# Optimization experiments

Measured on AMD Instinct MI355X. Metric: run time of the kernel, lower is better.

## Reference

```python
import jax, jax.numpy as jnp
import numpy as np

N, C, H, E = 10000, 128, 256, 320000
CUTOFF = 5.0
EPS = 1e-5


def _ln(x, g, b):
    mu = jnp.mean(x, axis=-1, keepdims=True)
    var = jnp.var(x, axis=-1, keepdims=True)
    return (x - mu) * jax.lax.rsqrt(var + EPS) * g + b


def setup_inputs() -> dict:
    key = jax.random.key(0)
    ks = jax.random.split(key, 24)

    def w(k, shape, fan_in):
        return (jax.random.normal(k, shape, dtype=jnp.float32) / np.sqrt(fan_in)).astype(jnp.float32)

    inp = {}
    inp["x"] = jax.random.normal(ks[0], (N, 3), dtype=jnp.float32)
    inp["h"] = jax.random.normal(ks[1], (N, C), dtype=jnp.float32)
    inp["edge_index"] = jax.random.randint(ks[2], (2, E), 0, N, dtype=jnp.int32)
    # edge_mlp: Linear(2C+1 -> H), SiLU, Linear(H -> H), SiLU
    inp["We1"] = w(ks[3], (2 * C + 1, H), 2 * C + 1); inp["be1"] = jnp.zeros((H,), jnp.float32)
    inp["We2"] = w(ks[4], (H, H), H);                inp["be2"] = jnp.zeros((H,), jnp.float32)
    # node_mlp: Linear(C+H -> H), SiLU, Linear(H -> C)
    inp["Wn1"] = w(ks[5], (C + H, H), C + H);        inp["bn1"] = jnp.zeros((H,), jnp.float32)
    inp["Wn2"] = w(ks[6], (H, C), H);                inp["bn2"] = jnp.zeros((C,), jnp.float32)
    # residual mlp: Linear(C -> H), SiLU, Dropout(eval), Linear(H -> C)
    inp["Wm1"] = w(ks[7], (C, H), C);                inp["bm1"] = jnp.zeros((H,), jnp.float32)
    inp["Wm2"] = w(ks[8], (H, C), H);                inp["bm2"] = jnp.zeros((C,), jnp.float32)
    # layernorms
    inp["g1"] = jnp.ones((C,), jnp.float32); inp["beta1"] = jnp.zeros((C,), jnp.float32)
    inp["g2"] = jnp.ones((C,), jnp.float32); inp["beta2"] = jnp.zeros((C,), jnp.float32)
    return inp


def reference(x, h, edge_index, We1, be1, We2, be2, Wn1, bn1, Wn2, bn2,
              Wm1, bm1, Wm2, bm2, g1, beta1, g2, beta2):
    row, col = edge_index[0], edge_index[1]

    h_res = h
    hn = _ln(h, g1, beta1)                              # [N, C]

    # ---- EGNN layer ----
    rel = x[row] - x[col]                               # [E, 3]
    dist = jnp.linalg.norm(rel, axis=-1, keepdims=True) # [E, 1]
    edge_in = jnp.concatenate([hn[row], hn[col], dist], axis=-1)  # [E, 2C+1]
    m = jax.nn.silu(edge_in @ We1 + be1)
    m = jax.nn.silu(m @ We2 + be2)                      # [E, H]

    d = dist[:, 0]
    Ccut = 0.5 * (jnp.cos(d * jnp.pi / CUTOFF) + 1.0)
    Ccut = Ccut * (d <= CUTOFF) * (d >= 0.0)
    m = m * Ccut[:, None]

    # mean-aggregate messages at target nodes (edge_index[1])
    sums = jax.ops.segment_sum(m, col, num_segments=N)          # [N, H]
    cnt = jax.ops.segment_sum(jnp.ones((m.shape[0],), m.dtype), col, num_segments=N)
    m_aggr = sums / jnp.maximum(cnt, 1.0)[:, None]

    hd = jax.nn.silu(jnp.concatenate([hn, m_aggr], axis=-1) @ Wn1 + bn1) @ Wn2 + bn2
    h_egnn = hn + hd

    h1 = h_res + h_egnn

    # ---- norm2 + MLP residual (dropout = identity in eval) ----
    h2 = _ln(h1, g2, beta2)
    h2 = jax.nn.silu(h2 @ Wm1 + bm1) @ Wm2 + bm2
    return h1 + h2
```

## Files before the change

### kernel.cpp

```cpp
#include <hip/hip_runtime.h>

#define NN 10000
#define CC 128
#define HH 256
#define EE 320000
#define ETILE 96
#define EBLOCKS 3334

typedef __bf16 bf16_t;
typedef __bf16 bf16x8 __attribute__((ext_vector_type(8)));
typedef __bf16 bf16x4 __attribute__((ext_vector_type(4)));
typedef float f32x4 __attribute__((ext_vector_type(4)));

__device__ __forceinline__ float silu_f(float v) {
#if __has_builtin(__builtin_amdgcn_rcpf)
  return v * __builtin_amdgcn_rcpf(1.0f + __expf(-v));
#else
  return v / (1.0f + __expf(-v));
#endif
}

template<int RE, int KD, int SA, int NT>
__device__ __forceinline__ void gemm_lg(const bf16_t* sAa, const bf16_t* __restrict__ BT,
                                        int nwavebase, int lr, int quad, f32x4 acc[RE][NT]) {
  for (int kk = 0; kk < KD; kk += 32) {
    bf16x8 a[RE]; bf16x8 b[NT];
#pragma unroll
    for (int re = 0; re < RE; re++)
      a[re] = *(const bf16x8*)(sAa + (re * 16 + lr) * SA + kk + quad * 8);
#pragma unroll
    for (int ce = 0; ce < NT; ce++)
      b[ce] = *(const bf16x8*)(BT + (size_t)(nwavebase + ce * 16 + lr) * KD + kk + quad * 8);
#pragma unroll
    for (int re = 0; re < RE; re++)
#pragma unroll
      for (int ce = 0; ce < NT; ce++)
        acc[re][ce] = __builtin_amdgcn_mfma_f32_16x16x32_bf16(a[re], b[ce], acc[re][ce], 0, 0, 0);
  }
}

__global__ __launch_bounds__(256) void prep_kernel(
    const float* __restrict__ We1, const float* __restrict__ We2,
    const float* __restrict__ Wn1, const float* __restrict__ Wn2,
    const float* __restrict__ Wm1, const float* __restrict__ Wm2,
    bf16_t* __restrict__ We1T, bf16_t* __restrict__ We2T,
    bf16_t* __restrict__ Wn1T, bf16_t* __restrict__ Wn2T,
    bf16_t* __restrict__ Wm1T, bf16_t* __restrict__ Wm2T,
    float* __restrict__ sums, int* __restrict__ cnt, uint4* __restrict__ edat) {
  int i = blockIdx.x * 256 + threadIdx.x;
  if (i < 327680) {
    const float* src; bf16_t* dst; int K, Nc, idx;
    if      (i < 65536)  { src = We1; dst = We1T; K = 256; Nc = 256; idx = i; }
    else if (i < 131072) { src = We2; dst = We2T; K = 256; Nc = 256; idx = i - 65536; }
    else if (i < 229376) { src = Wn1; dst = Wn1T; K = 384; Nc = 256; idx = i - 131072; }
    else if (i < 262144) { src = Wn2; dst = Wn2T; K = 256; Nc = 128; idx = i - 229376; }
    else if (i < 294912) { src = Wm1; dst = Wm1T; K = 128; Nc = 256; idx = i - 262144; }
    else                 { src = Wm2; dst = Wm2T; K = 256; Nc = 128; idx = i - 294912; }
    int n = idx / K, k = idx - n * K;
    dst[idx] = (bf16_t)src[(size_t)k * Nc + n];
  } else if (i < 327680 + 640000) {
    f32x4 z = {0.f, 0.f, 0.f, 0.f};
    ((f32x4*)sums)[i - 327680] = z;
  } else if (i < 327680 + 640000 + 2500) {
    int4 z = {0, 0, 0, 0};
    ((int4*)cnt)[i - 967680] = z;
  } else if (i < 327680 + 640000 + 2500 + 64) {
    uint4 z = {0u, 0u, 0u, 0u};
    edat[EE + (i - 970180)] = z;
  }
}

__global__ __launch_bounds__(256, 4) void node_pre_kernel(
    const float* __restrict__ h, const float* __restrict__ g1,
    const float* __restrict__ bt1,
    const bf16_t* __restrict__ We1T, const float* __restrict__ be1,
    bf16_t* __restrict__ hn16, bf16_t* __restrict__ PQ) {
  __shared__ __align__(16) bf16_t sHn[16 * 136];
  int tid = threadIdx.x;
  int lane = tid & 63, wave = tid >> 6;
  int lr = lane & 15, quad = lane >> 4;
  int n0 = blockIdx.x * 16;

  {
    int node = tid >> 4, c0 = (tid & 15) * 8;
    size_t base = (size_t)(n0 + node) * CC;
    f32x4 u0 = *(const f32x4*)(h + base + c0);
    f32x4 u1 = *(const f32x4*)(h + base + c0 + 4);
    float s = 0.f, sq = 0.f;
#pragma unroll
    for (int j = 0; j < 4; j++) { s += u0[j] + u1[j]; sq += u0[j] * u0[j] + u1[j] * u1[j]; }
#pragma unroll
    for (int o = 8; o > 0; o >>= 1) { s += __shfl_xor(s, o); sq += __shfl_xor(sq, o); }
    float mu = s * (1.0f / CC);
    float var = sq * (1.0f / CC) - mu * mu;
    float rs = rsqrtf(var + 1e-5f);
    f32x4 gg0 = *(const f32x4*)(g1 + c0), gg1 = *(const f32x4*)(g1 + c0 + 4);
    f32x4 bb0 = *(const f32x4*)(bt1 + c0), bb1 = *(const f32x4*)(bt1 + c0 + 4);
    bf16x8 ov;
#pragma unroll
    for (int j = 0; j < 4; j++) {
      ov[j] = (bf16_t)((u0[j] - mu) * rs * gg0[j] + bb0[j]);
      ov[j + 4] = (bf16_t)((u1[j] - mu) * rs * gg1[j] + bb1[j]);
    }
    *(bf16x8*)(sHn + node * 136 + c0) = ov;
    *(bf16x8*)(hn16 + base + c0) = ov;
  }
  __syncthreads();

  bool isQ = wave >= 2;
  int rbase = (wave & 1) * 128;
  int koff = isQ ? 128 : 0;
  f32x4 zf = {0.f, 0.f, 0.f, 0.f};
  f32x4 acc[8];
#pragma unroll
  for (int i = 0; i < 8; i++) acc[i] = zf;
  for (int kk = 0; kk < 128; kk += 32) {
    bf16x8 b = *(const bf16x8*)(sHn + lr * 136 + kk + quad * 8);
    bf16x8 a[8];
#pragma unroll
    for (int re = 0; re < 8; re++)
      a[re] = *(const bf16x8*)(We1T + (size_t)(rbase + re * 16 + lr) * 256 + koff + kk + quad * 8);
#pragma unroll
    for (int re = 0; re < 8; re++)
      acc[re] = __builtin_amdgcn_mfma_f32_16x16x32_bf16(a[re], b, acc[re], 0, 0, 0);
  }
#pragma unroll
  for (int re = 0; re < 8; re++) {
    int cb = rbase + re * 16 + quad * 4;
    f32x4 bb = isQ ? zf : *(const f32x4*)(be1 + cb);
    bf16x4 o;
#pragma unroll
    for (int r = 0; r < 4; r++) o[r] = (bf16_t)(acc[re][r] + bb[r]);
    *(bf16x4*)(PQ + (size_t)(n0 + lr) * 512 + (isQ ? 256 : 0) + cb) = o;
  }
}

__global__ __launch_bounds__(256) void count_kernel(const int* __restrict__ ei, int* __restrict__ cnt) {
  int e = blockIdx.x * 256 + threadIdx.x;
  atomicAdd(&cnt[ei[EE + e]], 1);
}

__global__ __launch_bounds__(1024) void scan_kernel(const int* __restrict__ cnt, int* __restrict__ cursor) {
  __shared__ int wsum[16];
  int tid = threadIdx.x, wave = tid >> 6, lane = tid & 63;
  int base = tid * 10;
  int v[10]; int S = 0;
#pragma unroll
  for (int j = 0; j < 10; j++) {
    int i = base + j;
    v[j] = (i < NN) ? cnt[i] : 0;
    S += v[j];
  }
  int s = S;
#pragma unroll
  for (int off = 1; off < 64; off <<= 1) { int t = __shfl_up(s, off); if (lane >= off) s += t; }
  if (lane == 63) wsum[wave] = s;
  __syncthreads();
  if (tid < 16) {
    int ws = wsum[tid];
#pragma unroll
    for (int off = 1; off < 16; off <<= 1) { int t = __shfl_up(ws, off); if (tid >= off) ws += t; }
    wsum[tid] = ws;
  }
  __syncthreads();
  int ex = ((wave > 0) ? wsum[wave - 1] : 0) + s - S;
#pragma unroll
  for (int j = 0; j < 10; j++) {
    int i = base + j;
    if (i < NN) cursor[i] = ex;
    ex += v[j];
  }
}

__global__ __launch_bounds__(256) void scatter_kernel(const int* __restrict__ ei,
                                                      const float* __restrict__ x,
                                                      int* __restrict__ cursor,
                                                      uint4* __restrict__ edat) {
  int e = blockIdx.x * 256 + threadIdx.x;
  int r = ei[e], c = ei[EE + e];
  float dx = x[3 * r] - x[3 * c];
  float dy = x[3 * r + 1] - x[3 * c + 1];
  float dz = x[3 * r + 2] - x[3 * c + 2];
  float d = sqrtf(dx * dx + dy * dy + dz * dz);
  float cc = (d <= 5.0f) ? 0.5f * (cosf(d * 0.6283185307179586f) + 1.0f) : 0.0f;
  int pos = atomicAdd(&cursor[c], 1);
  uint4 v = {(unsigned)r, (unsigned)c, __float_as_uint(d), __float_as_uint(cc)};
  edat[pos] = v;
}

__global__ __launch_bounds__(256, 3) void edge_mlp_kernel(
    const uint4* __restrict__ edat, const bf16_t* __restrict__ PQ,
    const float* __restrict__ We1last,
    const bf16_t* __restrict__ We2T, const float* __restrict__ be2,
    float* __restrict__ sums) {
  __shared__ __align__(16) bf16_t sM1[ETILE * 264];
  __shared__ int sRow[ETILE], sCol[ETILE];
  __shared__ float sD[ETILE], sCc[ETILE];
  __shared__ unsigned long long sMaskA;
  __shared__ unsigned sMaskB;
  int tid = threadIdx.x;
  int lane = tid & 63, wave = tid >> 6;
  int lr = lane & 15, quad = lane >> 4;
  int e0 = blockIdx.x * ETILE;

  if (tid < ETILE) {
    uint4 v = edat[e0 + tid];
    sRow[tid] = (int)v.x; sCol[tid] = (int)v.y;
    sD[tid] = __uint_as_float(v.z); sCc[tid] = __uint_as_float(v.w);
  }
  __syncthreads();

  if (tid < ETILE) {
    int fl = (tid > 0) && (sCol[tid] != sCol[tid - 1]);
    unsigned long long m = __ballot(fl);
    if (tid == 0) sMaskA = m;
    if (tid == 64) sMaskB = (unsigned)m;
  }

#pragma unroll
  for (int i = 0; i < ETILE * 32 / 256; i++) {
    int o = tid + i * 256;
    int e = o >> 5, q = o & 31;
    int k0 = q * 8;
    int row = sRow[e], col = sCol[e];
    float d = sD[e];
    bf16x8 pv = *(const bf16x8*)(PQ + (size_t)row * 512 + k0);
    bf16x8 qv = *(const bf16x8*)(PQ + (size_t)col * 512 + 256 + k0);
    f32x4 wl0 = *(const f32x4*)(We1last + k0);
    f32x4 wl1 = *(const f32x4*)(We1last + k0 + 4);
    bf16x8 m;
#pragma unroll
    for (int j = 0; j < 4; j++) {
      m[j] = (bf16_t)silu_f((float)pv[j] + (float)qv[j] + d * wl0[j]);
      m[j + 4] = (bf16_t)silu_f((float)pv[j + 4] + (float)qv[j + 4] + d * wl1[j]);
    }
    *(bf16x8*)(sM1 + e * 264 + k0) = m;
  }
  __syncthreads();

  f32x4 zf = {0.f, 0.f, 0.f, 0.f};
  f32x4 acc[6][4];
#pragma unroll
  for (int i = 0; i < 6; i++)
#pragma unroll
    for (int j = 0; j < 4; j++) acc[i][j] = zf;
  gemm_lg<6, 256, 264, 4>(sM1, We2T, wave * 64, lr, quad, acc);

  float be2v[4];
#pragma unroll
  for (int ce = 0; ce < 4; ce++) be2v[ce] = be2[wave * 64 + ce * 16 + lr];
#pragma unroll
  for (int re = 0; re < 6; re++) {
    f32x4 cc = *(const f32x4*)(sCc + re * 16 + quad * 4);
#pragma unroll
    for (int ce = 0; ce < 4; ce++)
#pragma unroll
      for (int r = 0; r < 4; r++)
        acc[re][ce][r] = silu_f(acc[re][ce][r] + be2v[ce]) * cc[r];
  }

  {
    unsigned long long mA = sMaskA;
    unsigned long long mB = (unsigned long long)sMaskB;
    int lo = 0;
    while (lo < ETILE) {
      int hi;
      if (lo < 63) {
        unsigned long long t = mA & (~0ull << (lo + 1));
        hi = t ? (__ffsll((long long)t) - 1)
               : (mB ? 64 + __ffsll((long long)mB) - 1 : ETILE);
      } else {
        unsigned long long t1 = mB & (~0ull << (lo - 63));
        hi = t1 ? 64 + __ffsll((long long)t1) - 1 : ETILE;
      }
      f32x4 tv = zf;
#pragma unroll
      for (int re = 0; re < 6; re++) {
        int t0 = re * 16, t1e = t0 + 16;
        if (t1e <= lo || t0 >= hi) continue;
        if (t0 >= lo && t1e <= hi) {
#pragma unroll
          for (int r = 0; r < 4; r++)
#pragma unroll
            for (int ce = 0; ce < 4; ce++)
              tv[ce] += acc[re][ce][r];
        } else {
          int eb = t0 + quad * 4;
#pragma unroll
          for (int r = 0; r < 4; r++) {
            int e = eb + r;
            bool in = (e >= lo) && (e < hi);
#pragma unroll
            for (int ce = 0; ce < 4; ce++)
              tv[ce] += in ? acc[re][ce][r] : 0.0f;
          }
        }
      }
#pragma unroll
      for (int ce = 0; ce < 4; ce++) {
        tv[ce] += __shfl_xor(tv[ce], 16);
        tv[ce] += __shfl_xor(tv[ce], 32);
      }
      if (quad == 0) {
        int colv = sCol[lo];
#pragma unroll
        for (int ce = 0; ce < 4; ce++)
          atomicAdd(&sums[(size_t)colv * HH + wave * 64 + ce * 16 + lr], tv[ce]);
      }
      lo = hi;
    }
  }
}

__global__ __launch_bounds__(256, 3) void node_fused_kernel(
    const float* __restrict__ h, const bf16_t* __restrict__ hn16,
    const float* __restrict__ sums, const int* __restrict__ cnt,
    const bf16_t* __restrict__ Wn1T, const float* __restrict__ bn1,
    const bf16_t* __restrict__ Wn2T, const float* __restrict__ bn2,
    const float* __restrict__ g2, const float* __restrict__ bt2,
    const bf16_t* __restrict__ Wm1T, const float* __restrict__ bm1,
    const bf16_t* __restrict__ Wm2T, const float* __restrict__ bm2,
    float* __restrict__ out) {
  __shared__ __align__(16) bf16_t sA1[16 * 392];
  __shared__ __align__(16) bf16_t sM[16 * 264];
  __shared__ __align__(16) float sH1[16 * 132];
  __shared__ __align__(16) bf16_t sLn[16 * 136];
  __shared__ float sRc[16];
  int tid = threadIdx.x;
  int lane = tid & 63, wave = tid >> 6;
  int lr = lane & 15, quad = lane >> 4;
  int n0 = blockIdx.x * 16;

  if (tid < 16) sRc[tid] = 1.0f / fmaxf((float)cnt[n0 + tid], 1.0f);
  __syncthreads();

#pragma unroll
  for (int i = 0; i < 3; i++) {
    int o = tid + i * 256;
    int e = o / 48, q = o - e * 48;
    int node = n0 + e;
    if (q < 16) {
      *(uint4*)(sA1 + e * 392 + q * 8) = *(const uint4*)(hn16 + (size_t)node * CC + q * 8);
    } else {
      float rc = sRc[e];
      const float* sp = sums + (size_t)node * HH + (q - 16) * 8;
      bf16x8 bv;
#pragma unroll
      for (int k2 = 0; k2 < 8; k2++) bv[k2] = (bf16_t)(sp[k2] * rc);
      *(bf16x8*)(sA1 + e * 392 + 128 + (q - 16) * 8) = bv;
    }
  }
  __syncthreads();

  f32x4 zf = {0.f, 0.f, 0.f, 0.f};
  {
    f32x4 acc[1][4];
#pragma unroll
    for (int j = 0; j < 4; j++) acc[0][j] = zf;
    gemm_lg<1, 384, 392, 4>(sA1, Wn1T, wave * 64, lr, quad, acc);
#pragma unroll
    for (int ce = 0; ce < 4; ce++) {
      int n = wave * 64 + ce * 16 + lr;
      float b1 = bn1[n];
#pragma unroll
      for (int r = 0; r < 4; r++)
        sM[(quad * 4 + r) * 264 + n] = (bf16_t)silu_f(acc[0][ce][r] + b1);
    }
  }
  __syncthreads();

  {
    f32x4 acc[1][2];
    acc[0][0] = zf; acc[0][1] = zf;
    gemm_lg<1, 256, 264, 2>(sM, Wn2T, wave * 32, lr, quad, acc);
#pragma unroll
    for (int ce = 0; ce < 2; ce++) {
      int n = wave * 32 + ce * 16 + lr;
      float b2 = bn2[n];
#pragma unroll
      for (int r = 0; r < 4; r++) {
        int node = quad * 4 + r;
        size_t idx = (size_t)(n0 + node) * CC + n;
        float hn_v = (float)sA1[node * 392 + n];
        sH1[node * 132 + n] = h[idx] + hn_v + acc[0][ce][r] + b2;
      }
    }
  }
  __syncthreads();

  {
    int node = tid >> 4, c0 = (tid & 15) * 8;
    f32x4 u0 = *(const f32x4*)(sH1 + node * 132 + c0);
    f32x4 u1 = *(const f32x4*)(sH1 + node * 132 + c0 + 4);
    float s = 0.f, sq = 0.f;
#pragma unroll
    for (int j = 0; j < 4; j++) { s += u0[j] + u1[j]; sq += u0[j] * u0[j] + u1[j] * u1[j]; }
#pragma unroll
    for (int o = 8; o > 0; o >>= 1) { s += __shfl_xor(s, o); sq += __shfl_xor(sq, o); }
    float mu = s * (1.0f / CC);
    float var = sq * (1.0f / CC) - mu * mu;
    float rs = rsqrtf(var + 1e-5f);
    f32x4 gg0 = *(const f32x4*)(g2 + c0), gg1 = *(const f32x4*)(g2 + c0 + 4);
    f32x4 bb0 = *(const f32x4*)(bt2 + c0), bb1 = *(const f32x4*)(bt2 + c0 + 4);
    bf16x8 ov;
#pragma unroll
    for (int j = 0; j < 4; j++) {
      ov[j] = (bf16_t)((u0[j] - mu) * rs * gg0[j] + bb0[j]);
      ov[j + 4] = (bf16_t)((u1[j] - mu) * rs * gg1[j] + bb1[j]);
    }
    *(bf16x8*)(sLn + node * 136 + c0) = ov;
  }
  __syncthreads();

  {
    f32x4 acc[1][4];
#pragma unroll
    for (int j = 0; j < 4; j++) acc[0][j] = zf;
    gemm_lg<1, 128, 136, 4>(sLn, Wm1T, wave * 64, lr, quad, acc);
#pragma unroll
    for (int ce = 0; ce < 4; ce++) {
      int n = wave * 64 + ce * 16 + lr;
      float b1 = bm1[n];
#pragma unroll
      for (int r = 0; r < 4; r++)
        sM[(quad * 4 + r) * 264 + n] = (bf16_t)silu_f(acc[0][ce][r] + b1);
    }
  }
  __syncthreads();

  {
    f32x4 acc[1][2];
    acc[0][0] = zf; acc[0][1] = zf;
    gemm_lg<1, 256, 264, 2>(sM, Wm2T, wave * 32, lr, quad, acc);
#pragma unroll
    for (int ce = 0; ce < 2; ce++) {
      int n = wave * 32 + ce * 16 + lr;
      float b2 = bm2[n];
#pragma unroll
      for (int r = 0; r < 4; r++) {
        int node = quad * 4 + r;
        size_t idx = (size_t)(n0 + node) * CC + n;
        out[idx] = sH1[node * 132 + n] + acc[0][ce][r] + b2;
      }
    }
  }
}

extern "C" void kernel_launch(void* const* d_in, const int* in_sizes, int n_in,
                              void* d_out, int out_size, void* d_ws, size_t ws_size,
                              hipStream_t stream) {
  const float* x    = (const float*)d_in[0];
  const float* h    = (const float*)d_in[1];
  const int*   ei   = (const int*)d_in[2];
  const float* We1  = (const float*)d_in[3];
  const float* be1  = (const float*)d_in[4];
  const float* We2  = (const float*)d_in[5];
  const float* be2  = (const float*)d_in[6];
  const float* Wn1  = (const float*)d_in[7];
  const float* bn1  = (const float*)d_in[8];
  const float* Wn2  = (const float*)d_in[9];
  const float* bn2  = (const float*)d_in[10];
  const float* Wm1  = (const float*)d_in[11];
  const float* bm1  = (const float*)d_in[12];
  const float* Wm2  = (const float*)d_in[13];
  const float* bm2  = (const float*)d_in[14];
  const float* g1   = (const float*)d_in[15];
  const float* bt1  = (const float*)d_in[16];
  const float* g2   = (const float*)d_in[17];
  const float* bt2  = (const float*)d_in[18];
  float* out = (float*)d_out;

  char* wp = (char*)d_ws;
  size_t off = 0;
  auto alloc = [&](size_t bytes) -> void* {
    void* p = wp + off;
    off = (off + bytes + 255) & ~(size_t)255;
    return p;
  };

  bf16_t* hn16   = (bf16_t*)alloc((size_t)NN * CC * 2);
  bf16_t* PQ     = (bf16_t*)alloc((size_t)NN * 512 * 2);
  float*  sums   = (float*)alloc((size_t)NN * HH * 4);
  int*    cnt    = (int*)alloc((size_t)NN * 4);
  int*    cursor = (int*)alloc((size_t)NN * 4);
  uint4*  edat   = (uint4*)alloc((size_t)(EBLOCKS * ETILE) * 16);
  bf16_t* We1T   = (bf16_t*)alloc(256 * 256 * 2);
  bf16_t* We2T   = (bf16_t*)alloc(256 * 256 * 2);
  bf16_t* Wn1T   = (bf16_t*)alloc(256 * 384 * 2);
  bf16_t* Wn2T   = (bf16_t*)alloc(128 * 256 * 2);
  bf16_t* Wm1T   = (bf16_t*)alloc(256 * 128 * 2);
  bf16_t* Wm2T   = (bf16_t*)alloc(128 * 256 * 2);

  prep_kernel<<<3791, 256, 0, stream>>>(We1, We2, Wn1, Wn2, Wm1, Wm2,
                                        We1T, We2T, Wn1T, Wn2T, Wm1T, Wm2T,
                                        sums, cnt, edat);

  node_pre_kernel<<<NN / 16, 256, 0, stream>>>(h, g1, bt1, We1T, be1, hn16, PQ);

  count_kernel<<<EE / 256, 256, 0, stream>>>(ei, cnt);
  scan_kernel<<<1, 1024, 0, stream>>>(cnt, cursor);
  scatter_kernel<<<EE / 256, 256, 0, stream>>>(ei, x, cursor, edat);

  edge_mlp_kernel<<<EBLOCKS, 256, 0, stream>>>(edat, PQ, We1 + 256 * 256,
                                               We2T, be2, sums);

  node_fused_kernel<<<NN / 16, 256, 0, stream>>>(h, hn16, sums, cnt,
                                                 Wn1T, bn1, Wn2T, bn2,
                                                 g2, bt2, Wm1T, bm1, Wm2T, bm2, out);
}
```

Measured before the change: 294.9 us.

## Split edge MLP K-loop into halves to shrink LDS; widen node tiles to 32

The edge MLP kernel now builds the first-layer activations and runs the second GEMM in two K halves of 128. This halves the shared-memory tile so more blocks can be resident, and the launch bound is raised from 3 to 5. The cost is an extra barrier and a recomputed index setup per half. Separately, the node kernel processes 32 nodes per block instead of 16, with bounds checks for the tail, so each weight fetch is reused across more rows at the price of lower occupancy.

New measurement: 861.2 us. 192% more time.

```diff
diff --git a/kernel.cpp b/kernel.cpp
--- a/kernel.cpp
+++ b/kernel.cpp
@@ -188,12 +188,12 @@
   edat[pos] = v;
 }
 
-__global__ __launch_bounds__(256, 3) void edge_mlp_kernel(
+__global__ __launch_bounds__(256, 5) void edge_mlp_kernel(
     const uint4* __restrict__ edat, const bf16_t* __restrict__ PQ,
     const float* __restrict__ We1last,
     const bf16_t* __restrict__ We2T, const float* __restrict__ be2,
     float* __restrict__ sums) {
-  __shared__ __align__(16) bf16_t sM1[ETILE * 264];
+  __shared__ __align__(16) bf16_t sM1[ETILE * 136];
   __shared__ int sRow[ETILE], sCol[ETILE];
   __shared__ float sD[ETILE], sCc[ETILE];
   __shared__ unsigned long long sMaskA;
@@ -217,34 +217,54 @@
     if (tid == 64) sMaskB = (unsigned)m;
   }
 
-#pragma unroll
-  for (int i = 0; i < ETILE * 32 / 256; i++) {
-    int o = tid + i * 256;
-    int e = o >> 5, q = o & 31;
-    int k0 = q * 8;
-    int row = sRow[e], col = sCol[e];
-    float d = sD[e];
-    bf16x8 pv = *(const bf16x8*)(PQ + (size_t)row * 512 + k0);
-    bf16x8 qv = *(const bf16x8*)(PQ + (size_t)col * 512 + 256 + k0);
-    f32x4 wl0 = *(const f32x4*)(We1last + k0);
-    f32x4 wl1 = *(const f32x4*)(We1last + k0 + 4);
-    bf16x8 m;
-#pragma unroll
-    for (int j = 0; j < 4; j++) {
-      m[j] = (bf16_t)silu_f((float)pv[j] + (float)qv[j] + d * wl0[j]);
-      m[j + 4] = (bf16_t)silu_f((float)pv[j + 4] + (float)qv[j + 4] + d * wl1[j]);
-    }
-    *(bf16x8*)(sM1 + e * 264 + k0) = m;
-  }
-  __syncthreads();
-
   f32x4 zf = {0.f, 0.f, 0.f, 0.f};
   f32x4 acc[6][4];
 #pragma unroll
   for (int i = 0; i < 6; i++)
 #pragma unroll
     for (int j = 0; j < 4; j++) acc[i][j] = zf;
-  gemm_lg<6, 256, 264, 4>(sM1, We2T, wave * 64, lr, quad, acc);
+
+#pragma unroll
+  for (int half = 0; half < 2; half++) {
+    int kbase = half * 128;
+    if (half) __syncthreads();
+
+#pragma unroll
+    for (int i = 0; i < 6; i++) {
+      int o = tid + i * 256;
+      int e = o >> 4, q = o & 15;
+      int k0 = q * 8;
+      int row = sRow[e], col = sCol[e];
+      float d = sD[e];
+      bf16x8 pv = *(const bf16x8*)(PQ + (size_t)row * 512 + kbase + k0);
+      bf16x8 qv = *(const bf16x8*)(PQ + (size_t)col * 512 + 256 + kbase + k0);
+      f32x4 wl0 = *(const f32x4*)(We1last + kbase + k0);
+      f32x4 wl1 = *(const f32x4*)(We1last + kbase + k0 + 4);
+      bf16x8 m;
+#pragma unroll
+      for (int j = 0; j < 4; j++) {
+        m[j] = (bf16_t)silu_f((float)pv[j] + (float)qv[j] + d * wl0[j]);
+        m[j + 4] = (bf16_t)silu_f((float)pv[j + 4] + (float)qv[j + 4] + d * wl1[j]);
+      }
+      *(bf16x8*)(sM1 + e * 136 + k0) = m;
+    }
+    __syncthreads();
+
+    for (int kk = 0; kk < 128; kk += 32) {
+      bf16x8 a[6]; bf16x8 b[4];
+#pragma unroll
+      for (int re = 0; re < 6; re++)
+        a[re] = *(const bf16x8*)(sM1 + (re * 16 + lr) * 136 + kk + quad * 8);
+#pragma unroll
+      for (int ce = 0; ce < 4; ce++)
+        b[ce] = *(const bf16x8*)(We2T + (size_t)(wave * 64 + ce * 16 + lr) * 256 + kbase + kk + quad * 8);
+#pragma unroll
+      for (int re = 0; re < 6; re++)
+#pragma unroll
+        for (int ce = 0; ce < 4; ce++)
+          acc[re][ce] = __builtin_amdgcn_mfma_f32_16x16x32_bf16(a[re], b[ce], acc[re][ce], 0, 0, 0);
+    }
+  }
 
   float be2v[4];
 #pragma unroll
@@ -312,7 +332,7 @@
   }
 }
 
-__global__ __launch_bounds__(256, 3) void node_fused_kernel(
+__global__ __launch_bounds__(256, 2) void node_fused_kernel(
     const float* __restrict__ h, const bf16_t* __restrict__ hn16,
     const float* __restrict__ sums, const int* __restrict__ cnt,
     const bf16_t* __restrict__ Wn1T, const float* __restrict__ bn1,
@@ -321,32 +341,39 @@
     const bf16_t* __restrict__ Wm1T, const float* __restrict__ bm1,
     const bf16_t* __restrict__ Wm2T, const float* __restrict__ bm2,
     float* __restrict__ out) {
-  __shared__ __align__(16) bf16_t sA1[16 * 392];
-  __shared__ __align__(16) bf16_t sM[16 * 264];
-  __shared__ __align__(16) float sH1[16 * 132];
-  __shared__ __align__(16) bf16_t sLn[16 * 136];
-  __shared__ float sRc[16];
+  __shared__ __align__(16) bf16_t sA1[32 * 392];
+  __shared__ __align__(16) bf16_t sM[32 * 264];
+  __shared__ __align__(16) float sH1[32 * 132];
+  __shared__ __align__(16) bf16_t sLn[32 * 136];
+  __shared__ float sRc[32];
   int tid = threadIdx.x;
   int lane = tid & 63, wave = tid >> 6;
   int lr = lane & 15, quad = lane >> 4;
-  int n0 = blockIdx.x * 16;
-
-  if (tid < 16) sRc[tid] = 1.0f / fmaxf((float)cnt[n0 + tid], 1.0f);
-  __syncthreads();
-
-#pragma unroll
-  for (int i = 0; i < 3; i++) {
+  int n0 = blockIdx.x * 32;
+
+  if (tid < 32) {
+    int node = n0 + tid;
+    sRc[tid] = (node < NN) ? 1.0f / fmaxf((float)cnt[node], 1.0f) : 0.0f;
+  }
+  __syncthreads();
+
+#pragma unroll
+  for (int i = 0; i < 6; i++) {
     int o = tid + i * 256;
     int e = o / 48, q = o - e * 48;
     int node = n0 + e;
     if (q < 16) {
-      *(uint4*)(sA1 + e * 392 + q * 8) = *(const uint4*)(hn16 + (size_t)node * CC + q * 8);
+      uint4 v = {0u, 0u, 0u, 0u};
+      if (node < NN) v = *(const uint4*)(hn16 + (size_t)node * CC + q * 8);
+      *(uint4*)(sA1 + e * 392 + q * 8) = v;
     } else {
-      float rc = sRc[e];
-      const float* sp = sums + (size_t)node * HH + (q - 16) * 8;
-      bf16x8 bv;
-#pragma unroll
-      for (int k2 = 0; k2 < 8; k2++) bv[k2] = (bf16_t)(sp[k2] * rc);
+      bf16x8 bv = {};
+      if (node < NN) {
+        float rc = sRc[e];
+        const float* sp = sums + (size_t)node * HH + (q - 16) * 8;
+#pragma unroll
+        for (int k2 = 0; k2 < 8; k2++) bv[k2] = (bf16_t)(sp[k2] * rc);
+      }
       *(bf16x8*)(sA1 + e * 392 + 128 + (q - 16) * 8) = bv;
     }
   }
@@ -354,94 +381,117 @@
 
   f32x4 zf = {0.f, 0.f, 0.f, 0.f};
   {
-    f32x4 acc[1][4];
-#pragma unroll
-    for (int j = 0; j < 4; j++) acc[0][j] = zf;
-    gemm_lg<1, 384, 392, 4>(sA1, Wn1T, wave * 64, lr, quad, acc);
+    f32x4 acc[2][4];
+#pragma unroll
+    for (int i = 0; i < 2; i++)
+#pragma unroll
+      for (int j = 0; j < 4; j++) acc[i][j] = zf;
+    gemm_lg<2, 384, 392, 4>(sA1, Wn1T, wave * 64, lr, quad, acc);
 #pragma unroll
     for (int ce = 0; ce < 4; ce++) {
       int n = wave * 64 + ce * 16 + lr;
       float b1 = bn1[n];
 #pragma unroll
-      for (int r = 0; r < 4; r++)
-        sM[(quad * 4 + r) * 264 + n] = (bf16_t)silu_f(acc[0][ce][r] + b1);
-    }
-  }
-  __syncthreads();
-
-  {
-    f32x4 acc[1][2];
-    acc[0][0] = zf; acc[0][1] = zf;
-    gemm_lg<1, 256, 264, 2>(sM, Wn2T, wave * 32, lr, quad, acc);
+      for (int re = 0; re < 2; re++)
+#pragma unroll
+        for (int r = 0; r < 4; r++)
+          sM[(re * 16 + quad * 4 + r) * 264 + n] = (bf16_t)silu_f(acc[re][ce][r] + b1);
+    }
+  }
+  __syncthreads();
+
+  {
+    f32x4 acc[2][2];
+#pragma unroll
+    for (int i = 0; i < 2; i++) { acc[i][0] = zf; acc[i][1] = zf; }
+    gemm_lg<2, 256, 264, 2>(sM, Wn2T, wave * 32, lr, quad, acc);
 #pragma unroll
     for (int ce = 0; ce < 2; ce++) {
       int n = wave * 32 + ce * 16 + lr;
       float b2 = bn2[n];
 #pragma unroll
-      for (int r = 0; r < 4; r++) {
-        int node = quad * 4 + r;
-        size_t idx = (size_t)(n0 + node) * CC + n;
-        float hn_v = (float)sA1[node * 392 + n];
-        sH1[node * 132 + n] = h[idx] + hn_v + acc[0][ce][r] + b2;
-      }
-    }
-  }
-  __syncthreads();
-
-  {
-    int node = tid >> 4, c0 = (tid & 15) * 8;
-    f32x4 u0 = *(const f32x4*)(sH1 + node * 132 + c0);
-    f32x4 u1 = *(const f32x4*)(sH1 + node * 132 + c0 + 4);
+      for (int re = 0; re < 2; re++)
+#pragma unroll
+        for (int r = 0; r < 4; r++) {
+          int node = re * 16 + quad * 4 + r;
+          float hv = 0.f;
+          if (n0 + node < NN) hv = h[(size_t)(n0 + node) * CC + n];
+          sH1[node * 132 + n] = hv + (float)sA1[node * 392 + n] + acc[re][ce][r] + b2;
+        }
+    }
+  }
+  __syncthreads();
+
+  {
+    int node = tid >> 3, c0 = (tid & 7) * 16;
+    f32x4 u[4];
     float s = 0.f, sq = 0.f;
 #pragma unroll
-    for (int j = 0; j < 4; j++) { s += u0[j] + u1[j]; sq += u0[j] * u0[j] + u1[j] * u1[j]; }
-#pragma unroll
-    for (int o = 8; o > 0; o >>= 1) { s += __shfl_xor(s, o); sq += __shfl_xor(sq, o); }
+    for (int j = 0; j < 4; j++) {
+      u[j] = *(const f32x4*)(sH1 + node * 132 + c0 + j * 4);
+#pragma unroll
+      for (int r = 0; r < 4; r++) { s += u[j][r]; sq += u[j][r] * u[j][r]; }
+    }
+    s += __shfl_xor(s, 1); sq += __shfl_xor(sq, 1);
+    s += __shfl_xor(s, 2); sq += __shfl_xor(sq, 2);
+    s += __shfl_xor(s, 4); sq += __shfl_xor(sq, 4);
     float mu = s * (1.0f / CC);
     float var = sq * (1.0f / CC) - mu * mu;
     float rs = rsqrtf(var + 1e-5f);
-    f32x4 gg0 = *(const f32x4*)(g2 + c0), gg1 = *(const f32x4*)(g2 + c0 + 4);
-    f32x4 bb0 = *(const f32x4*)(bt2 + c0), bb1 = *(const f32x4*)(bt2 + c0 + 4);
-    bf16x8 ov;
-#pragma unroll
-    for (int j = 0; j < 4; j++) {
-      ov[j] = (bf16_t)((u0[j] - mu) * rs * gg0[j] + bb0[j]);
-      ov[j + 4] = (bf16_t)((u1[j] - mu) * rs * gg1[j] + bb1[j]);
-    }
-    *(bf16x8*)(sLn + node * 136 + c0) = ov;
-  }
-  __syncthreads();
-
-  {
-    f32x4 acc[1][4];
-#pragma unroll
-    for (int j = 0; j < 4; j++) acc[0][j] = zf;
-    gemm_lg<1, 128, 136, 4>(sLn, Wm1T, wave * 64, lr, quad, acc);
+#pragma unroll
+    for (int j2 = 0; j2 < 2; j2++) {
+      f32x4 gg0 = *(const f32x4*)(g2 + c0 + j2 * 8);
+      f32x4 gg1 = *(const f32x4*)(g2 + c0 + j2 * 8 + 4);
+      f32x4 bb0 = *(const f32x4*)(bt2 + c0 + j2 * 8);
+      f32x4 bb1 = *(const f32x4*)(bt2 + c0 + j2 * 8 + 4);
+      bf16x8 ov;
+#pragma unroll
+      for (int r = 0; r < 4; r++) {
+        ov[r] = (bf16_t)((u[j2 * 2][r] - mu) * rs * gg0[r] + bb0[r]);
+        ov[r + 4] = (bf16_t)((u[j2 * 2 + 1][r] - mu) * rs * gg1[r] + bb1[r]);
+      }
+      *(bf16x8*)(sLn + node * 136 + c0 + j2 * 8) = ov;
+    }
+  }
+  __syncthreads();
+
+  {
+    f32x4 acc[2][4];
+#pragma unroll
+    for (int i = 0; i < 2; i++)
+#pragma unroll
+      for (int j = 0; j < 4; j++) acc[i][j] = zf;
+    gemm_lg<2, 128, 136, 4>(sLn, Wm1T, wave * 64, lr, quad, acc);
 #pragma unroll
     for (int ce = 0; ce < 4; ce++) {
       int n = wave * 64 + ce * 16 + lr;
       float b1 = bm1[n];
 #pragma unroll
-      for (int r = 0; r < 4; r++)
-        sM[(quad * 4 + r) * 264 + n] = (bf16_t)silu_f(acc[0][ce][r] + b1);
-    }
-  }
-  __syncthreads();
-
-  {
-    f32x4 acc[1][2];
-    acc[0][0] = zf; acc[0][1] = zf;
-    gemm_lg<1, 256, 264, 2>(sM, Wm2T, wave * 32, lr, quad, acc);
+      for (int re = 0; re < 2; re++)
+#pragma unroll
+        for (int r = 0; r < 4; r++)
+          sM[(re * 16 + quad * 4 + r) * 264 + n] = (bf16_t)silu_f(acc[re][ce][r] + b1);
+    }
+  }
+  __syncthreads();
+
+  {
+    f32x4 acc[2][2];
+#pragma unroll
+    for (int i = 0; i < 2; i++) { acc[i][0] = zf; acc[i][1] = zf; }
+    gemm_lg<2, 256, 264, 2>(sM, Wm2T, wave * 32, lr, quad, acc);
 #pragma unroll
     for (int ce = 0; ce < 2; ce++) {
       int n = wave * 32 + ce * 16 + lr;
       float b2 = bm2[n];
 #pragma unroll
-      for (int r = 0; r < 4; r++) {
-        int node = quad * 4 + r;
-        size_t idx = (size_t)(n0 + node) * CC + n;
-        out[idx] = sH1[node * 132 + n] + acc[0][ce][r] + b2;
-      }
+      for (int re = 0; re < 2; re++)
+#pragma unroll
+        for (int r = 0; r < 4; r++) {
+          int node = re * 16 + quad * 4 + r;
+          if (n0 + node < NN)
+            out[(size_t)(n0 + node) * CC + n] = sH1[node * 132 + n] + acc[re][ce][r] + b2;
+        }
     }
   }
 }
@@ -504,7 +554,7 @@
   edge_mlp_kernel<<<EBLOCKS, 256, 0, stream>>>(edat, PQ, We1 + 256 * 256,
                                                We2T, be2, sums);
 
-  node_fused_kernel<<<NN / 16, 256, 0, stream>>>(h, hn16, sums, cnt,
-                                                 Wn1T, bn1, Wn2T, bn2,
-                                                 g2, bt2, Wm1T, bm1, Wm2T, bm2, out);
-}
+  node_fused_kernel<<<(NN + 31) / 32, 256, 0, stream>>>(h, hn16, sums, cnt,
+                                                        Wn1T, bn1, Wn2T, bn2,
+                                                        g2, bt2, Wm1T, bm1, Wm2T, bm2, out);
+}
```
